# Kernel optimization log

Hardware: AMD Instinct MI355X
Metric: run time of the kernel (lower is better)

## Reference

```python
import jax, jax.numpy as jnp
import numpy as np

N_NODES = 50000
N_EDGES = 800000
NUM_IN, NUM_OUT, NUM_HID, NUM_MSG = 1, 1, 30, 200


def _linear_params(key, fan_in, fan_out):
    k1, k2 = jax.random.split(key)
    s = 1.0 / np.sqrt(fan_in)
    W = jax.random.uniform(k1, (fan_in, fan_out), jnp.float32, -s, s)
    b = jax.random.uniform(k2, (fan_out,), jnp.float32, -s, s)
    return W, b


def _layer_params(key, c_in, c_out, c_msg):
    ks = jax.random.split(key, 4)
    W1, b1 = _linear_params(ks[0], c_in, c_out)          # lin_1
    Wm1, bm1 = _linear_params(ks[1], 2 * c_in + 2, c_msg)  # mlp[0]
    Wm2, bm2 = _linear_params(ks[2], c_msg, c_in)          # mlp[2]
    W2, b2 = _linear_params(ks[3], c_in, c_out)          # lin_2
    return W1, b1, Wm1, bm1, Wm2, bm2, W2, b2


def setup_inputs() -> dict:
    key = jax.random.key(0)
    ks = jax.random.split(key, 6)
    features = jax.random.normal(ks[0], (N_NODES, NUM_IN), jnp.float32)
    edges = jax.random.randint(ks[1], (2, N_EDGES), 0, N_NODES, jnp.int64)
    weights = jax.random.normal(ks[2], (N_EDGES, 2), jnp.float32)
    inp = {"features": features, "edges": edges, "weights": weights}
    names = ["W1", "b1", "Wm1", "bm1", "Wm2", "bm2", "W2", "b2"]
    for suf, kk, (ci, co) in zip(["d", "h", "o"], ks[3:6],
                                 [(NUM_IN, NUM_HID), (NUM_HID, NUM_HID), (NUM_HID, NUM_OUT)]):
        ps = _layer_params(kk, ci, co, NUM_MSG)
        for nm, p in zip(names, ps):
            inp[f"{nm}_{suf}"] = p
    return inp


def _mpd(x, src, dst, ea, W1, b1, Wm1, bm1, Wm2, bm2, W2, b2):
    # PyG default flow source_to_target: x_j = x[src], x_i = x[dst], aggregate to dst
    xi = x[dst]
    xj = x[src]
    tmp = jnp.concatenate([xi, xj, ea], axis=1)            # [E, 2*in+2]
    h = jax.nn.relu(tmp @ Wm1 + bm1)                       # [E, msg]
    m = h @ Wm2 + bm2                                      # [E, in]
    msg = (m * (xi - xj)) @ W2 + b2                        # [E, out]
    agg = jax.ops.segment_sum(msg, dst, num_segments=x.shape[0])
    return agg + x @ W1 + b1


def reference(features, edges, weights,
              W1_d, b1_d, Wm1_d, bm1_d, Wm2_d, bm2_d, W2_d, b2_d,
              W1_h, b1_h, Wm1_h, bm1_h, Wm2_h, bm2_h, W2_h, b2_h,
              W1_o, b1_o, Wm1_o, bm1_o, Wm2_o, bm2_o, W2_o, b2_o):
    src, dst = edges[0], edges[1]
    x = jax.nn.relu(_mpd(features, src, dst, weights,
                         W1_d, b1_d, Wm1_d, bm1_d, Wm2_d, bm2_d, W2_d, b2_d))
    for _ in range(3):
        x = jax.nn.relu(_mpd(x, src, dst, weights,
                             W1_h, b1_h, Wm1_h, bm1_h, Wm2_h, bm2_h, W2_h, b2_h))
    return _mpd(x, src, dst, weights,
                W1_o, b1_o, Wm1_o, bm1_o, Wm2_o, bm2_o, W2_o, b2_o)
```

## Files before the change

kernel.cpp:

```cpp
#include <hip/hip_runtime.h>

#define N_NODES 50000
#define N_EDGES 800000
#define C_MSG 200

typedef __bf16 bf16;
typedef __attribute__((ext_vector_type(8))) __bf16 bf16x8;
typedef __attribute__((ext_vector_type(4))) float f32x4;

static __device__ __forceinline__ unsigned int pk_bf16(float a, float b) {
    union { bf16 h[2]; unsigned int u; } cv;
    cv.h[0] = (bf16)a; cv.h[1] = (bf16)b;
    return cv.u;
}

static __device__ __forceinline__ f32x4 MF(bf16x8 a, bf16x8 b, f32x4 c) {
    return __builtin_amdgcn_mfma_f32_16x16x32_bf16(a, b, c, 0, 0, 0);
}

static __device__ void dev_pack_wm1(int tid, const float* W, const float* bm1,
                                    bf16* out) {
    int i = tid & 7, lane = (tid >> 3) & 63, rest = tid >> 9;
    int kt = rest % 2, t = rest / 2;
    int k = kt * 32 + ((lane >> 4) * 8) + i;
    int c = lane & 15;
    int n = (t < 12) ? ((t >> 1) * 32 + 2 * c + (t & 1)) : (192 + c);
    float v = 0.f;
    if (n < C_MSG) {
        if (k < 30)       v = W[k * C_MSG + n];
        else if (k == 30) v = bm1[n];
        else if (k >= 32) v = W[(k - 2) * C_MSG + n];
    }
    out[tid] = (bf16)v;
}

static __device__ void dev_pack_wm2(int tid, const float* W, const float* bm2,
                                    bf16* out) {
    int i = tid & 7, lane = (tid >> 3) & 63, rest = tid >> 9;
    int kt = rest % 7, nt = rest / 7;
    int k = kt * 32 + ((lane >> 4) * 8) + i;
    int n = 2 * (lane & 15) + nt;
    float v = 0.f;
    if (n < 30) {
        if (k < C_MSG)       v = W[k * 30 + n];
        else if (k == C_MSG) v = bm2[n];
    }
    out[tid] = (bf16)v;
}

static __device__ void dev_pack_w2h(int tid, const float* W, const float* b2,
                                    bf16* out) {
    int i = tid & 7, lane = (tid >> 3) & 63, nt = tid >> 9;
    int k = ((lane >> 4) * 8) + i;
    int n = 2 * (lane & 15) + nt;
    float v = 0.f;
    if (n < 30) {
        if (k < 30)       v = W[k * 30 + n];
        else if (k == 30) v = b2[n];
    }
    out[tid] = (bf16)v;
}

static __device__ void dev_pack_w2o(int tid, const float* W, const float* b2,
                                    bf16* out) {
    int i = tid & 7, lane = (tid >> 3) & 63;
    int k = ((lane >> 4) * 8) + i;
    int n = lane & 15;
    float v = 0.f;
    if (n == 0) {
        if (k < 30)       v = W[k];
        else if (k == 30) v = b2[0];
    }
    out[tid] = (bf16)v;
}

static __device__ void dev_pack_sel(int tid, bf16* out) {
    int i = tid & 7, lane = (tid >> 3) & 63, f = tid >> 9;
    int kt = f >> 1, nt = f & 1;
    int kloc = ((lane >> 4) * 8) + i;
    int n = 2 * (lane & 15) + nt;
    float v = (kloc == n && n < 30) ? ((kt & 1) ? -1.f : 1.f) : 0.f;
    out[tid] = (bf16)v;
}

__global__ __launch_bounds__(256) void setup_a(
    const int* __restrict__ dst, int* __restrict__ counts,
    const float* __restrict__ Wm1_h, const float* __restrict__ bm1_h,
    const float* __restrict__ Wm1_o, const float* __restrict__ bm1_o,
    const float* __restrict__ Wm2_h, const float* __restrict__ bm2_h,
    const float* __restrict__ Wm2_o, const float* __restrict__ bm2_o,
    const float* __restrict__ W2_h,  const float* __restrict__ b2_h,
    const float* __restrict__ W2_o,  const float* __restrict__ b2_o,
    const float* __restrict__ Wm1_d,
    bf16* __restrict__ Wm1B_h, bf16* __restrict__ Wm1B_o,
    bf16* __restrict__ Wm2B_h, bf16* __restrict__ Wm2B_o,
    bf16* __restrict__ W2B_h,  bf16* __restrict__ W2B_o,
    bf16* __restrict__ SelB,   float* __restrict__ Wm1T_d,
    const float* __restrict__ features, const float* __restrict__ W1_d,
    const float* __restrict__ b1_d, float* __restrict__ bufA) {
    int b = blockIdx.x, t = threadIdx.x;
    if (b < 3125) {
        int e = b * 256 + t;
        if (e < N_EDGES) atomicAdd(&counts[dst[e]], 1);
    } else if (b < 3311) {
        int pb = b - 3125;
        if (pb < 52)       dev_pack_wm1(pb * 256 + t, Wm1_h, bm1_h, Wm1B_h);
        else if (pb < 104) dev_pack_wm1((pb - 52) * 256 + t, Wm1_o, bm1_o, Wm1B_o);
        else if (pb < 132) dev_pack_wm2((pb - 104) * 256 + t, Wm2_h, bm2_h, Wm2B_h);
        else if (pb < 160) dev_pack_wm2((pb - 132) * 256 + t, Wm2_o, bm2_o, Wm2B_o);
        else if (pb < 164) dev_pack_w2h((pb - 160) * 256 + t, W2_h, b2_h, W2B_h);
        else if (pb < 166) dev_pack_w2o((pb - 164) * 256 + t, W2_o, b2_o, W2B_o);
        else if (pb < 182) dev_pack_sel((pb - 166) * 256 + t, SelB);
        else {
            int i = (pb - 182) * 256 + t;
            if (i < C_MSG * 4) Wm1T_d[i] = Wm1_d[(i & 3) * C_MSG + (i >> 2)];
        }
    } else {
        int n = (b - 3311) * 256 + t;
        if (n < N_NODES) {
            float xv = features[n];
            for (int o = 0; o < 30; ++o)
                bufA[n * 30 + o] = fmaf(xv, W1_d[o], b1_d[o]);
        }
    }
}

__global__ __launch_bounds__(256) void scan_kernel(const int* __restrict__ counts,
                                                   int* __restrict__ offsets,
                                                   int* __restrict__ cursor) {
    __shared__ int ws[4];
    const int b = blockIdx.x, t = threadIdx.x;
    const int lane = t & 63, wv = t >> 6;
    int acc = 0;
    for (int i = t; i < b * 256; i += 256) acc += counts[i];
#pragma unroll
    for (int d = 32; d > 0; d >>= 1) acc += __shfl_xor(acc, d);
    if (lane == 0) ws[wv] = acc;
    __syncthreads();
    int base = ws[0] + ws[1] + ws[2] + ws[3];
    __syncthreads();
    int i = b * 256 + t;
    int v = (i < N_NODES) ? counts[i] : 0;
    int inc = v;
#pragma unroll
    for (int d = 1; d < 64; d <<= 1) {
        int u = __shfl_up(inc, d);
        if (lane >= d) inc += u;
    }
    if (lane == 63) ws[wv] = inc;
    __syncthreads();
    int waveoff = 0;
    for (int k = 0; k < wv; ++k) waveoff += ws[k];
    int excl = base + waveoff + inc - v;
    if (i < N_NODES) { offsets[i] = excl; cursor[i] = excl; }
    if (i == N_NODES - 1) offsets[N_NODES] = excl + v;
}

__global__ __launch_bounds__(256) void scatter_kernel(
    const int* __restrict__ src, const int* __restrict__ dst,
    const float* __restrict__ ew, int* __restrict__ cursor,
    int4* __restrict__ edata, float2* __restrict__ ewp) {
    int e = blockIdx.x * 256 + threadIdx.x;
    if (e < N_EDGES) {
        int d = dst[e];
        float e0 = ew[2 * e], e1 = ew[2 * e + 1];
        int p = atomicAdd(&cursor[d], 1);
        edata[p] = make_int4(src[e], d, (int)pk_bf16(e0, e1), e);
        ewp[p] = make_float2(e0, e1);
    }
}

__global__ __launch_bounds__(256) void edge_d_kernel(
    const float* __restrict__ x, const int4* __restrict__ edata,
    const float2* __restrict__ ewp,
    const float* __restrict__ Wm1T, const float* __restrict__ bm1,
    const float* __restrict__ Wm2, const float* __restrict__ bm2,
    const float* __restrict__ W2, const float* __restrict__ b2, bf16* __restrict__ msg)
{
    __shared__ float sw[C_MSG * 6 + 1];
    for (int i = threadIdx.x; i < C_MSG * 6 + 1; i += 256) {
        float v;
        if (i < C_MSG * 4)            v = Wm1T[i];
        else if (i < C_MSG * 5)       v = bm1[i - C_MSG * 4];
        else if (i < C_MSG * 6)       v = Wm2[i - C_MSG * 5];
        else                          v = bm2[0];
        sw[i] = v;
    }
    __syncthreads();

    int t = blockIdx.x * 256 + threadIdx.x;
    int4 ed = edata[t];
    float xi = x[ed.y], xj = x[ed.x];
    float2 e01 = ewp[t];
    float e0 = e01.x, e1 = e01.y;
    float m = sw[C_MSG * 6];
#pragma unroll 4
    for (int j = 0; j < C_MSG; ++j) {
        const float* wr = sw + j * 4;
        float h = sw[C_MSG * 4 + j];
        h = fmaf(xi, wr[0], h);
        h = fmaf(xj, wr[1], h);
        h = fmaf(e0, wr[2], h);
        h = fmaf(e1, wr[3], h);
        h = fmaxf(h, 0.f);
        m = fmaf(h, sw[C_MSG * 5 + j], m);
    }
    float md = m * (xi - xj);
    for (int o = 0; o < 15; ++o) {
        float f0 = fmaf(md, W2[2 * o], b2[2 * o]);
        float f1 = fmaf(md, W2[2 * o + 1], b2[2 * o + 1]);
        *(unsigned int*)(msg + (size_t)t * 32 + 2 * o) = pk_bf16(f0, f1);
    }
}


#define LOAD_FRAGS(P, ED) do {                                                \
    const bf16* rd_ = xc + (size_t)(ED).y * 64 + quad * 8;                    \
    const bf16* rs_ = xc + (size_t)(ED).x * 64 + quad * 8;                    \
    P##A0 = *(const bf16x8*)(rd_);                                            \
    P##a2 = *(const bf16x8*)(rd_ + 32);                                       \
    P##A1 = *(const bf16x8*)(rs_);                                            \
    P##a3 = *(const bf16x8*)(rs_ + 32);                                       \
} while (0)

#define COMPUTE_TILE(P, EDZ, EBASE) do {                                      \
    if (quad == 3) {                                                          \
        union { unsigned int u; bf16 b[2]; } cv_;                             \
        cv_.u = (unsigned int)(EDZ);                                          \
        P##A1[6] = cv_.b[0];                                                  \
        P##A1[7] = cv_.b[1];                                                  \
    }                                                                         \
    __builtin_amdgcn_s_setprio(1);                                            \
               \
    f32x4 m0_ = {0.f,0.f,0.f,0.f}, m1_ = {0.f,0.f,0.f,0.f};                   \
    _Pragma("unroll")                                                         \
    for (int p_ = 0; p_ < 6; ++p_) {                                          \
        char* cb_ = (p_ & 1) ? cB : cA;                                       \
        const bf16* Wf_ = Wm1L + (4 * p_) * 512 + lane * 8;                   \
        bf16x8 be0_ = *(const bf16x8*)(Wf_);                                  \
        bf16x8 be1_ = *(const bf16x8*)(Wf_ + 512);                            \
        bf16x8 bo0_ = *(const bf16x8*)(Wf_ + 1024);                           \
        bf16x8 bo1_ = *(const bf16x8*)(Wf_ + 1536);                           \
        f32x4 ae_ = {0.f,0.f,0.f,0.f}, ao_ = {0.f,0.f,0.f,0.f};               \
        ae_ = MF(P##A0, be0_, ae_);                                           \
        ae_ = MF(P##A1, be1_, ae_);                                           \
        ao_ = MF(P##A0, bo0_, ao_);                                           \
        ao_ = MF(P##A1, bo1_, ao_);                                           \
        _Pragma("unroll")                                                     \
        for (int rg_ = 0; rg_ < 4; ++rg_) {                                   \
            int row_ = row0 + rg_, wb_ = 4 * col;                             \
            unsigned int u_ = pk_bf16(fmaxf(ae_[rg_],0.f), fmaxf(ao_[rg_],0.f)); \
            *(unsigned int*)(cb_ + row_ * 64 + ((wb_ & 48) ^ ((row_ & 3) << 4)) \
                             + (wb_ & 15)) = u_;                              \
        }                                                                     \
        bf16x8 a_ = *(const bf16x8*)(cb_ + col * 64 +                         \
                                     ((quad << 4) ^ ((col & 3) << 4)));       \
        m0_ = MF(a_, *(const bf16x8*)(Wm2L + p_ * 512 + lane * 8), m0_);      \
        m1_ = MF(a_, *(const bf16x8*)(Wm2L + (7 + p_) * 512 + lane * 8), m1_);\
    }                                                                         \
    {     \
        const bf16* Wf_ = Wm1L + 24 * 512 + lane * 8;                         \
        bf16x8 b0_ = *(const bf16x8*)(Wf_);                                   \
        bf16x8 b1_ = *(const bf16x8*)(Wf_ + 512);                             \
        f32x4 acc_ = {0.f,0.f,0.f,0.f};                                       \
        acc_ = MF(P##A0, b0_, acc_);                                          \
        acc_ = MF(P##A1, b1_, acc_);                                          \
        if (col < 8) {                                                        \
            _Pragma("unroll")                                                 \
            for (int rg_ = 0; rg_ < 4; ++rg_) {                               \
                int row_ = row0 + rg_;                                        \
                *(bf16*)(cP + row_ * 64 + ((row_ & 3) << 4) + 2 * col) =      \
                    (bf16)fmaxf(acc_[rg_], 0.f);                              \
            }                                                                 \
        }                                                                     \
        bf16x8 a_ = *(const bf16x8*)(cP + col * 64 +                          \
                                     ((quad << 4) ^ ((col & 3) << 4)));       \
        m0_ = MF(a_, *(const bf16x8*)(Wm2L + 6 * 512 + lane * 8), m0_);       \
        m1_ = MF(a_, *(const bf16x8*)(Wm2L + 13 * 512 + lane * 8), m1_);      \
    }                                                                         \
          \
    f32x4 dc0_ = {0.f,0.f,0.f,0.f}, dc1_ = {0.f,0.f,0.f,0.f};                 \
    dc0_ = MF(P##A0, *(const bf16x8*)(SelB + (size_t)0*512 + lane*8), dc0_);  \
    dc1_ = MF(P##A0, *(const bf16x8*)(SelB + (size_t)1*512 + lane*8), dc1_);  \
    dc0_ = MF(P##A1, *(const bf16x8*)(SelB + (size_t)2*512 + lane*8), dc0_);  \
    dc1_ = MF(P##A1, *(const bf16x8*)(SelB + (size_t)3*512 + lane*8), dc1_);  \
    dc0_ = MF(P##a2, *(const bf16x8*)(SelB + (size_t)4*512 + lane*8), dc0_);  \
    dc1_ = MF(P##a2, *(const bf16x8*)(SelB + (size_t)5*512 + lane*8), dc1_);  \
    dc0_ = MF(P##a3, *(const bf16x8*)(SelB + (size_t)6*512 + lane*8), dc0_);  \
    dc1_ = MF(P##a3, *(const bf16x8*)(SelB + (size_t)7*512 + lane*8), dc1_);  \
                                   \
    _Pragma("unroll")                                                         \
    for (int rg_ = 0; rg_ < 4; ++rg_) {                                       \
        int row_ = row0 + rg_, wb_ = 4 * col;                                 \
        unsigned int u_ = (col == 15) ? pk_bf16(1.f, 0.f)                     \
                        : pk_bf16(m0_[rg_]*dc0_[rg_], m1_[rg_]*dc1_[rg_]);    \
        *(unsigned int*)(cA + row_ * 64 + ((wb_ & 48) ^ ((row_ & 3) << 4))    \
                         + (wb_ & 15)) = u_;                                  \
    }                                                                         \
    bf16x8 am_ = *(const bf16x8*)(cA + col * 64 +                             \
                                  ((quad << 4) ^ ((col & 3) << 4)));          \
                                      \
    if (COUT == 30) {                                                         \
        f32x4 c0_ = {0.f,0.f,0.f,0.f}, c1_ = {0.f,0.f,0.f,0.f};               \
        c0_ = MF(am_, *(const bf16x8*)(W2B + lane*8), c0_);                   \
        c1_ = MF(am_, *(const bf16x8*)(W2B + 512 + lane*8), c1_);             \
        __builtin_amdgcn_s_setprio(0);                                        \
        _Pragma("unroll")                                                     \
        for (int rg_ = 0; rg_ < 4; ++rg_)                                     \
            *(unsigned int*)(msg + (size_t)((EBASE) + row0 + rg_)*32 + 2*col) = \
                pk_bf16(c0_[rg_], c1_[rg_]);                                  \
    } else {                                                                  \
                  \
        f32x4 c0_ = {0.f,0.f,0.f,0.f};                                        \
        c0_ = MF(am_, *(const bf16x8*)(W2B + lane*8), c0_);                   \
        __builtin_amdgcn_s_setprio(0);                                        \
        if (col == 0) {                                                       \
            union { bf16 h[4]; unsigned long long u; } pk4_;                  \
            _Pragma("unroll")                                                 \
            for (int rg_ = 0; rg_ < 4; ++rg_) pk4_.h[rg_] = (bf16)c0_[rg_];   \
            *(unsigned long long*)(msg + ((EBASE) + row0)) = pk4_.u;          \
        }                                                                     \
    }                                                                         \
} while (0)

template<int COUT>
__global__ __launch_bounds__(256, 3) void edge_mfma(
    const bf16* __restrict__ xc, const int4* __restrict__ edata,
    const bf16* __restrict__ Wm1B, const bf16* __restrict__ SelB,
    const bf16* __restrict__ Wm2B, const bf16* __restrict__ W2B,
    bf16* __restrict__ msg)
{
    __shared__ __align__(16) bf16 smem[26624];
    bf16* Wm1L = smem;
    bf16* Wm2L = smem + 13312;

    const int tid = threadIdx.x, w = tid >> 6, lane = tid & 63;
    const int col = lane & 15, quad = lane >> 4, row0 = quad * 4;
    const int myrow = w * 16;

    const int nblk = gridDim.x;
    const int q = nblk >> 3, r = nblk & 7;
    const int xcd = blockIdx.x & 7, idx = blockIdx.x >> 3;
    const int sbid = (xcd < r) ? (xcd * (q + 1) + idx)
                               : (r * (q + 1) + (xcd - r) * q + idx);
    const int blk = sbid * 256;

    const int eoff = myrow + col;
    int4 ed0 = edata[blk + 0 * 64 + eoff];
    int4 ed1 = edata[blk + 1 * 64 + eoff];
    int4 ed2 = edata[blk + 2 * 64 + eoff];
    int4 ed3 = edata[blk + 3 * 64 + eoff];

#pragma unroll
    for (int i = 0; i < 10; ++i) {
        int idxs = tid + i * 256;
        bf16x8 v = (idxs < 1664) ? *((const bf16x8*)Wm1B + idxs)
                                 : *((const bf16x8*)Wm2B + (idxs - 1664));
        *((bf16x8*)smem + idxs) = v;
    }
    __syncthreads();

    char* cbase = (char*)(smem + 20480 + w * 1536);
    char* cA = cbase;
    char* cB = cbase + 1024;
    char* cP = cbase + 2048;

    if (lane < 48) {
        int rr = lane / 3, s = 1 + (lane - rr * 3);
        bf16x8 z = {};
        if (s == 1) z[0] = (bf16)1.f;
        *(bf16x8*)(cP + rr * 64 + ((s << 4) ^ ((rr & 3) << 4))) = z;
    }

    bf16x8 pA0, pA1, pa2, pa3, qA0, qA1, qa2, qa3;
    LOAD_FRAGS(p, ed0);
    LOAD_FRAGS(q, ed1);

    COMPUTE_TILE(p, ed0.z, blk + 0 * 64 + myrow);
    LOAD_FRAGS(p, ed2);
    COMPUTE_TILE(q, ed1.z, blk + 1 * 64 + myrow);
    LOAD_FRAGS(q, ed3);
    COMPUTE_TILE(p, ed2.z, blk + 2 * 64 + myrow);
    COMPUTE_TILE(q, ed3.z, blk + 3 * 64 + myrow);
}

template<int CNEXT>
__global__ __launch_bounds__(256) void agg_fused(
    const bf16* __restrict__ msg, const int* __restrict__ offsets,
    const float* __restrict__ bufc,
    const float* __restrict__ W1n, const float* __restrict__ b1n,
    float* __restrict__ bufn,
    bf16* __restrict__ xc) {
    int gh = (blockIdx.x * 256 + threadIdx.x) >> 4;
    int lane = threadIdx.x & 15;
    int s0 = offsets[gh], s1 = offsets[gh + 1];
    float r0 = 0.f, r1 = 0.f;
    if (lane < 15) {
        float v0 = 0.f, v1 = 0.f;
        const unsigned int* mp =
            (const unsigned int*)(msg + (size_t)s0 * 32 + lane * 2);
        int cnt = s1 - s0, j = 0;
        for (; j + 8 <= cnt; j += 8) {
            unsigned int u0 = mp[(size_t)(j + 0) * 16];
            unsigned int u1 = mp[(size_t)(j + 1) * 16];
            unsigned int u2 = mp[(size_t)(j + 2) * 16];
            unsigned int u3 = mp[(size_t)(j + 3) * 16];
            unsigned int u4 = mp[(size_t)(j + 4) * 16];
            unsigned int u5 = mp[(size_t)(j + 5) * 16];
            unsigned int u6 = mp[(size_t)(j + 6) * 16];
            unsigned int u7 = mp[(size_t)(j + 7) * 16];
            union { unsigned int u; bf16 b[2]; } c0, c1, c2, c3, c4, c5, c6, c7;
            c0.u = u0; c1.u = u1; c2.u = u2; c3.u = u3;
            c4.u = u4; c5.u = u5; c6.u = u6; c7.u = u7;
            v0 += (float)c0.b[0]; v1 += (float)c0.b[1];
            v0 += (float)c1.b[0]; v1 += (float)c1.b[1];
            v0 += (float)c2.b[0]; v1 += (float)c2.b[1];
            v0 += (float)c3.b[0]; v1 += (float)c3.b[1];
            v0 += (float)c4.b[0]; v1 += (float)c4.b[1];
            v0 += (float)c5.b[0]; v1 += (float)c5.b[1];
            v0 += (float)c6.b[0]; v1 += (float)c6.b[1];
            v0 += (float)c7.b[0]; v1 += (float)c7.b[1];
        }
        for (; j + 4 <= cnt; j += 4) {
            unsigned int u0 = mp[(size_t)(j + 0) * 16];
            unsigned int u1 = mp[(size_t)(j + 1) * 16];
            unsigned int u2 = mp[(size_t)(j + 2) * 16];
            unsigned int u3 = mp[(size_t)(j + 3) * 16];
            union { unsigned int u; bf16 b[2]; } c0, c1, c2, c3;
            c0.u = u0; c1.u = u1; c2.u = u2; c3.u = u3;
            v0 += (float)c0.b[0]; v1 += (float)c0.b[1];
            v0 += (float)c1.b[0]; v1 += (float)c1.b[1];
            v0 += (float)c2.b[0]; v1 += (float)c2.b[1];
            v0 += (float)c3.b[0]; v1 += (float)c3.b[1];
        }
        for (; j < cnt; ++j) {
            union { unsigned int u; bf16 b[2]; } cv;
            cv.u = mp[(size_t)j * 16];
            v0 += (float)cv.b[0]; v1 += (float)cv.b[1];
        }
        float f0 = bufc[(size_t)gh * 30 + 2 * lane] + v0;
        float f1 = bufc[(size_t)gh * 30 + 2 * lane + 1] + v1;
        r0 = fmaxf(f0, 0.f);
        r1 = fmaxf(f1, 0.f);
        bf16 h0 = (bf16)r0, h1 = (bf16)r1;
        union { bf16 h[2]; unsigned int u; } hi;
        hi.h[0] = h0; hi.h[1] = h1;
        *(unsigned int*)(xc + (size_t)gh * 64 + 2 * lane) = hi.u;
        *(unsigned int*)(xc + (size_t)gh * 64 + 32 + 2 * lane) =
            pk_bf16(r0 - (float)h0, r1 - (float)h1);
    } else {
        *(unsigned int*)(xc + (size_t)gh * 64 + 30) = pk_bf16(1.f, 0.f);
        *(unsigned int*)(xc + (size_t)gh * 64 + 62) = 0u;
    }
    if (CNEXT == 30) {
        float acc0 = 0.f, acc1 = 0.f;
        if (lane < 15) { acc0 = b1n[2 * lane]; acc1 = b1n[2 * lane + 1]; }
        for (int k2 = 0; k2 < 15; ++k2) {
            float rk0 = __shfl(r0, k2, 16);
            float rk1 = __shfl(r1, k2, 16);
            if (lane < 15) {
                const float* w0 = W1n + (2 * k2) * 30 + 2 * lane;
                const float* w1 = W1n + (2 * k2 + 1) * 30 + 2 * lane;
                acc0 = fmaf(rk0, w0[0], acc0);
                acc1 = fmaf(rk0, w0[1], acc1);
                acc0 = fmaf(rk1, w1[0], acc0);
                acc1 = fmaf(rk1, w1[1], acc1);
            }
        }
        if (lane < 15) {
            bufn[(size_t)gh * 30 + 2 * lane] = acc0;
            bufn[(size_t)gh * 30 + 2 * lane + 1] = acc1;
        }
    } else {
        float acc = b1n[0];
        for (int k2 = 0; k2 < 15; ++k2) {
            float rk0 = __shfl(r0, k2, 16);
            float rk1 = __shfl(r1, k2, 16);
            acc = fmaf(rk0, W1n[2 * k2], acc);
            acc = fmaf(rk1, W1n[2 * k2 + 1], acc);
        }
        if (lane == 0) bufn[gh] = acc;
    }
}

__global__ __launch_bounds__(256) void agg_last(const bf16* __restrict__ msg1,
                                                const int* __restrict__ offsets,
                                                float* __restrict__ out) {
    int gh = (blockIdx.x * 256 + threadIdx.x) >> 5;
    int lane = threadIdx.x & 31;
    int s0 = offsets[gh], s1 = offsets[gh + 1];
    float v = 0.f;
    for (int j = s0 + lane; j < s1; j += 32) v += (float)msg1[j];
#pragma unroll
    for (int o = 16; o > 0; o >>= 1) v += __shfl_xor(v, o);
    if (lane == 0) out[gh] += v;
}

extern "C" void kernel_launch(void* const* d_in, const int* in_sizes, int n_in,
                              void* d_out, int out_size, void* d_ws, size_t ws_size,
                              hipStream_t stream) {
    const float* features = (const float*)d_in[0];
    const int*   edges    = (const int*)d_in[1];
    const float* ew       = (const float*)d_in[2];

    const float* W1_d  = (const float*)d_in[3];
    const float* b1_d  = (const float*)d_in[4];
    const float* Wm1_d = (const float*)d_in[5];
    const float* bm1_d = (const float*)d_in[6];
    const float* Wm2_d = (const float*)d_in[7];
    const float* bm2_d = (const float*)d_in[8];
    const float* W2_d  = (const float*)d_in[9];
    const float* b2_d  = (const float*)d_in[10];

    const float* W1_h  = (const float*)d_in[11];
    const float* b1_h  = (const float*)d_in[12];
    const float* Wm1_h = (const float*)d_in[13];
    const float* bm1_h = (const float*)d_in[14];
    const float* Wm2_h = (const float*)d_in[15];
    const float* bm2_h = (const float*)d_in[16];
    const float* W2_h  = (const float*)d_in[17];
    const float* b2_h  = (const float*)d_in[18];

    const float* W1_o  = (const float*)d_in[19];
    const float* b1_o  = (const float*)d_in[20];
    const float* Wm1_o = (const float*)d_in[21];
    const float* bm1_o = (const float*)d_in[22];
    const float* Wm2_o = (const float*)d_in[23];
    const float* bm2_o = (const float*)d_in[24];
    const float* W2_o  = (const float*)d_in[25];
    const float* b2_o  = (const float*)d_in[26];

    const int* src = edges;
    const int* dst = edges + N_EDGES;
    float* out = (float*)d_out;

    char* p = (char*)d_ws;
    auto alloc = [&](size_t bytes) { char* r = p; p += (bytes + 63) & ~(size_t)63; return r; };
    float* bufA    = (float*)alloc((size_t)N_NODES * 30 * 4);
    float* bufB    = (float*)alloc((size_t)N_NODES * 30 * 4);
    bf16*  msg     = (bf16*) alloc((size_t)N_EDGES * 32 * 2);
    bf16*  xc      = (bf16*) alloc((size_t)N_NODES * 64 * 2);
    int*   counts  = (int*)  alloc((size_t)N_NODES * 4);
    int*   offsets = (int*)  alloc((size_t)(N_NODES + 1) * 4);
    int*   cursor  = (int*)  alloc((size_t)N_NODES * 4);
    int4*  edata   = (int4*) alloc((size_t)N_EDGES * 16);
    float2* ewp    = (float2*)alloc((size_t)N_EDGES * 8);
    float* Wm1T_d  = (float*)alloc((size_t)C_MSG * 4 * 4);
    bf16*  Wm1B_h  = (bf16*) alloc((size_t)26 * 512 * 2);
    bf16*  Wm1B_o  = (bf16*) alloc((size_t)26 * 512 * 2);
    bf16*  Wm2B_h  = (bf16*) alloc((size_t)14 * 512 * 2);
    bf16*  Wm2B_o  = (bf16*) alloc((size_t)14 * 512 * 2);
    bf16*  W2B_h   = (bf16*) alloc((size_t)2 * 512 * 2);
    bf16*  W2B_o   = (bf16*) alloc((size_t)1 * 512 * 2);
    bf16*  SelB    = (bf16*) alloc((size_t)8 * 512 * 2);

    hipMemsetAsync(counts, 0, (size_t)N_NODES * 4, stream);
    setup_a<<<3507, 256, 0, stream>>>(dst, counts,
        Wm1_h, bm1_h, Wm1_o, bm1_o, Wm2_h, bm2_h, Wm2_o, bm2_o,
        W2_h, b2_h, W2_o, b2_o, Wm1_d,
        Wm1B_h, Wm1B_o, Wm2B_h, Wm2B_o, W2B_h, W2B_o, SelB, Wm1T_d,
        features, W1_d, b1_d, bufA);
    scan_kernel<<<(N_NODES + 255) / 256, 256, 0, stream>>>(counts, offsets, cursor);
    scatter_kernel<<<N_EDGES / 256, 256, 0, stream>>>(src, dst, ew, cursor, edata, ewp);

    dim3 tb(256);
    dim3 eb_mfma(N_EDGES / 256);
    dim3 eb_valu(N_EDGES / 256);
    dim3 ab16(N_NODES * 16 / 256);
    dim3 ab32(N_NODES * 32 / 256);

    edge_d_kernel<<<eb_valu, tb, 0, stream>>>(features, edata, ewp,
        Wm1T_d, bm1_d, Wm2_d, bm2_d, W2_d, b2_d, msg);
    agg_fused<30><<<ab16, tb, 0, stream>>>(msg, offsets, bufA, W1_h, b1_h, bufB, xc);

    edge_mfma<30><<<eb_mfma, tb, 0, stream>>>(xc, edata,
        Wm1B_h, SelB, Wm2B_h, W2B_h, msg);
    agg_fused<30><<<ab16, tb, 0, stream>>>(msg, offsets, bufB, W1_h, b1_h, bufA, xc);

    edge_mfma<30><<<eb_mfma, tb, 0, stream>>>(xc, edata,
        Wm1B_h, SelB, Wm2B_h, W2B_h, msg);
    agg_fused<30><<<ab16, tb, 0, stream>>>(msg, offsets, bufA, W1_h, b1_h, bufB, xc);

    edge_mfma<30><<<eb_mfma, tb, 0, stream>>>(xc, edata,
        Wm1B_h, SelB, Wm2B_h, W2B_h, msg);
    agg_fused<1><<<ab16, tb, 0, stream>>>(msg, offsets, bufB, W1_o, b1_o, out, xc);

    edge_mfma<1><<<eb_mfma, tb, 0, stream>>>(xc, edata,
        Wm1B_o, SelB, Wm2B_o, W2B_o, msg);
    agg_last<<<ab32, tb, 0, stream>>>(msg, offsets, out);
}
```

Baseline: 581.6 us.

## Read Wm2 fragments from global memory to cut LDS and raise occupancy

Wm2 is no longer staged in shared memory. Its MFMA B-fragments are loaded straight from global memory (through the caches), which shrinks the LDS footprint from about 52KB to 38KB per block and lets launch bounds ask for 4 blocks per CU instead of 3. The change also drops the XCD-aware block remapping and the s_setprio bracketing around the MFMA chain. The cost is extra global/L2 traffic and latency on every tile's Wm2 loads, and tighter register limits at the higher occupancy.

```diff
diff --git a/kernel.cpp b/kernel.cpp
--- a/kernel.cpp
+++ b/kernel.cpp
@@ -230,7 +230,6 @@
         P##A1[6] = cv_.b[0];                                                  \
         P##A1[7] = cv_.b[1];                                                  \
     }                                                                         \
-    __builtin_amdgcn_s_setprio(1);                                            \
                \
     f32x4 m0_ = {0.f,0.f,0.f,0.f}, m1_ = {0.f,0.f,0.f,0.f};                   \
     _Pragma("unroll")                                                         \
@@ -255,8 +254,8 @@
         }                                                                     \
         bf16x8 a_ = *(const bf16x8*)(cb_ + col * 64 +                         \
                                      ((quad << 4) ^ ((col & 3) << 4)));       \
-        m0_ = MF(a_, *(const bf16x8*)(Wm2L + p_ * 512 + lane * 8), m0_);      \
-        m1_ = MF(a_, *(const bf16x8*)(Wm2L + (7 + p_) * 512 + lane * 8), m1_);\
+        m0_ = MF(a_, *(const bf16x8*)(Wm2B + (size_t)p_ * 512 + lane * 8), m0_); \
+        m1_ = MF(a_, *(const bf16x8*)(Wm2B + (size_t)(7 + p_) * 512 + lane * 8), m1_); \
     }                                                                         \
     {     \
         const bf16* Wf_ = Wm1L + 24 * 512 + lane * 8;                         \
@@ -275,8 +274,8 @@
         }                                                                     \
         bf16x8 a_ = *(const bf16x8*)(cP + col * 64 +                          \
                                      ((quad << 4) ^ ((col & 3) << 4)));       \
-        m0_ = MF(a_, *(const bf16x8*)(Wm2L + 6 * 512 + lane * 8), m0_);       \
-        m1_ = MF(a_, *(const bf16x8*)(Wm2L + 13 * 512 + lane * 8), m1_);      \
+        m0_ = MF(a_, *(const bf16x8*)(Wm2B + (size_t)6 * 512 + lane * 8), m0_); \
+        m1_ = MF(a_, *(const bf16x8*)(Wm2B + (size_t)13 * 512 + lane * 8), m1_); \
     }                                                                         \
           \
     f32x4 dc0_ = {0.f,0.f,0.f,0.f}, dc1_ = {0.f,0.f,0.f,0.f};                 \
@@ -304,7 +303,6 @@
         f32x4 c0_ = {0.f,0.f,0.f,0.f}, c1_ = {0.f,0.f,0.f,0.f};               \
         c0_ = MF(am_, *(const bf16x8*)(W2B + lane*8), c0_);                   \
         c1_ = MF(am_, *(const bf16x8*)(W2B + 512 + lane*8), c1_);             \
-        __builtin_amdgcn_s_setprio(0);                                        \
         _Pragma("unroll")                                                     \
         for (int rg_ = 0; rg_ < 4; ++rg_)                                     \
             *(unsigned int*)(msg + (size_t)((EBASE) + row0 + rg_)*32 + 2*col) = \
@@ -313,7 +311,6 @@
                   \
         f32x4 c0_ = {0.f,0.f,0.f,0.f};                                        \
         c0_ = MF(am_, *(const bf16x8*)(W2B + lane*8), c0_);                   \
-        __builtin_amdgcn_s_setprio(0);                                        \
         if (col == 0) {                                                       \
             union { bf16 h[4]; unsigned long long u; } pk4_;                  \
             _Pragma("unroll")                                                 \
@@ -324,26 +321,19 @@
 } while (0)
 
 template<int COUT>
-__global__ __launch_bounds__(256, 3) void edge_mfma(
+__global__ __launch_bounds__(256, 4) void edge_mfma(
     const bf16* __restrict__ xc, const int4* __restrict__ edata,
     const bf16* __restrict__ Wm1B, const bf16* __restrict__ SelB,
     const bf16* __restrict__ Wm2B, const bf16* __restrict__ W2B,
     bf16* __restrict__ msg)
 {
-    __shared__ __align__(16) bf16 smem[26624];
+    __shared__ __align__(16) bf16 smem[19456];
     bf16* Wm1L = smem;
-    bf16* Wm2L = smem + 13312;
 
     const int tid = threadIdx.x, w = tid >> 6, lane = tid & 63;
     const int col = lane & 15, quad = lane >> 4, row0 = quad * 4;
     const int myrow = w * 16;
-
-    const int nblk = gridDim.x;
-    const int q = nblk >> 3, r = nblk & 7;
-    const int xcd = blockIdx.x & 7, idx = blockIdx.x >> 3;
-    const int sbid = (xcd < r) ? (xcd * (q + 1) + idx)
-                               : (r * (q + 1) + (xcd - r) * q + idx);
-    const int blk = sbid * 256;
+    const int blk = blockIdx.x * 256;
 
     const int eoff = myrow + col;
     int4 ed0 = edata[blk + 0 * 64 + eoff];
@@ -352,24 +342,23 @@
     int4 ed3 = edata[blk + 3 * 64 + eoff];
 
 #pragma unroll
-    for (int i = 0; i < 10; ++i) {
-        int idxs = tid + i * 256;
-        bf16x8 v = (idxs < 1664) ? *((const bf16x8*)Wm1B + idxs)
-                                 : *((const bf16x8*)Wm2B + (idxs - 1664));
-        *((bf16x8*)smem + idxs) = v;
+    for (int i = 0; i < 7; ++i) {
+        int idx = tid + i * 256;
+        if (idx < 1664)
+            *((bf16x8*)smem + idx) = *((const bf16x8*)Wm1B + idx);
     }
     __syncthreads();
 
-    char* cbase = (char*)(smem + 20480 + w * 1536);
+    char* cbase = (char*)(smem + 13312 + w * 1536);
     char* cA = cbase;
     char* cB = cbase + 1024;
     char* cP = cbase + 2048;
 
     if (lane < 48) {
-        int rr = lane / 3, s = 1 + (lane - rr * 3);
+        int r = lane / 3, s = 1 + (lane - r * 3);
         bf16x8 z = {};
         if (s == 1) z[0] = (bf16)1.f;
-        *(bf16x8*)(cP + rr * 64 + ((s << 4) ^ ((rr & 3) << 4))) = z;
+        *(bf16x8*)(cP + r * 64 + ((s << 4) ^ ((r & 3) << 4))) = z;
     }
 
     bf16x8 pA0, pA1, pa2, pa3, qA0, qA1, qa2, qa3;
```

Result: slower. 683.3 us (+17.5%).
